# Performance work log

Measured on AMD Instinct MI355X. Metric: run time of the kernel, lower is better.

## Reference

```python
import jax, jax.numpy as jnp
import numpy as np

N_NODES = 100000
N_EDGES = 1600000
IN_F = 128
OUT_F = 32


def setup_inputs() -> dict:
    key = jax.random.key(0)
    k1, k2, k3, k4, k5, k6 = jax.random.split(key, 6)
    x = jax.random.normal(k1, (N_NODES, IN_F), dtype=jnp.float32)
    adj_row = jax.random.randint(k2, (N_EDGES,), 0, N_NODES, dtype=jnp.int64)
    adj_col = jax.random.randint(k3, (N_EDGES,), 0, N_NODES, dtype=jnp.int64)
    adj_val = jax.random.uniform(k4, (N_EDGES,), dtype=jnp.float32)
    weight = jax.random.normal(k5, (IN_F, OUT_F), dtype=jnp.float32) * (1.0 / np.sqrt(IN_F))
    bias = jax.random.normal(k6, (OUT_F,), dtype=jnp.float32)
    return {"x": x, "adj_row": adj_row, "adj_col": adj_col,
            "adj_val": adj_val, "weight": weight, "bias": bias}


def reference(x, adj_row, adj_col, adj_val, weight, bias):
    # support = input @ W   -> [N, out]
    support = x @ weight
    # spmm(adj, support): out[r] = sum_e val[e] * support[col[e]] for edges with row[e]==r
    gathered = adj_val[:, None] * support[adj_col]  # [E, out]
    out = jax.ops.segment_sum(gathered, adj_row, num_segments=N_NODES)
    return out + bias
```

## Files before the change

kernel.cpp:

```cpp
#include <hip/hip_runtime.h>
#include <stdint.h>

#define N_NODES 100000
#define N_EDGES 1600000
#define IN_F 128
#define OUT_F 32

#define RB 64
#define NB 1563
#define ABLK 256
#define EPA (N_EDGES / ABLK)
#define NTOT (NB * ABLK)
#define NSA NB
#define CAP 1536
#define MTILES (N_NODES / 16)
#define GEMM_BLKS ((MTILES + 7) / 8)

typedef __attribute__((ext_vector_type(8))) short bf16x8;
typedef __attribute__((ext_vector_type(4))) float f32x4;

__device__ __forceinline__ float bf2f(unsigned short u) {
    return __uint_as_float(((uint32_t)u) << 16);
}
__device__ __forceinline__ unsigned short f2bf(float x) {
    const uint32_t b = __float_as_uint(x);
    return (unsigned short)((b + 0x7fffu + ((b >> 16) & 1u)) >> 16);
}

__global__ __launch_bounds__(512) void gcn_gemm_count(const float* __restrict__ x,
                                                      const float* __restrict__ w,
                                                      unsigned short* __restrict__ support,
                                                      const int* __restrict__ row,
                                                      int* __restrict__ count) {
    __shared__ unsigned short wt[OUT_F][IN_F + 8];
    __shared__ int h[NB];
    const int tid = threadIdx.x;

    if (blockIdx.x < GEMM_BLKS) {
        #pragma unroll
        for (int i = tid; i < IN_F * OUT_F; i += 512) {
            const int k = i >> 5, f = i & 31;
            wt[f][k] = f2bf(w[i]);
        }
        __syncthreads();

        const int wv = tid >> 6;
        const int lane = tid & 63;
        const int rowT = blockIdx.x * 8 + wv;
        if (rowT >= MTILES) return;
        const int row0 = rowT * 16;

        const int mrow = lane & 15;
        const int kg = lane >> 4;
        const int kb = kg * 8;

        bf16x8 bfrag[4][2];
        #pragma unroll
        for (int ks = 0; ks < 4; ++ks) {
            #pragma unroll
            for (int nt = 0; nt < 2; ++nt) {
                bfrag[ks][nt] = *reinterpret_cast<const bf16x8*>(
                    &wt[mrow + nt * 16][ks * 32 + kb]);
            }
        }

        f32x4 acc0 = {0.f, 0.f, 0.f, 0.f};
        f32x4 acc1 = {0.f, 0.f, 0.f, 0.f};
        const float* xr = &x[(size_t)(row0 + mrow) * IN_F];
        #pragma unroll
        for (int ks = 0; ks < 4; ++ks) {
            const float4 a0 = *reinterpret_cast<const float4*>(&xr[ks * 32 + kb]);
            const float4 a1 = *reinterpret_cast<const float4*>(&xr[ks * 32 + kb + 4]);
            bf16x8 af;
            af[0] = (short)f2bf(a0.x); af[1] = (short)f2bf(a0.y);
            af[2] = (short)f2bf(a0.z); af[3] = (short)f2bf(a0.w);
            af[4] = (short)f2bf(a1.x); af[5] = (short)f2bf(a1.y);
            af[6] = (short)f2bf(a1.z); af[7] = (short)f2bf(a1.w);
            acc0 = __builtin_amdgcn_mfma_f32_16x16x32_bf16(af, bfrag[ks][0], acc0, 0, 0, 0);
            acc1 = __builtin_amdgcn_mfma_f32_16x16x32_bf16(af, bfrag[ks][1], acc1, 0, 0, 0);
        }
        #pragma unroll
        for (int r = 0; r < 4; ++r) {
            const int orow = row0 + kg * 4 + r;
            support[(size_t)orow * OUT_F + mrow]      = f2bf(acc0[r]);
            support[(size_t)orow * OUT_F + mrow + 16] = f2bf(acc1[r]);
        }
    } else {
        const int b = blockIdx.x - GEMM_BLKS;
        for (int i = tid; i < NB; i += 512) h[i] = 0;
        __syncthreads();
        const int e0 = b * EPA;
        for (int i = tid; i < EPA; i += 512)
            atomicAdd(&h[row[e0 + i] >> 6], 1);
        __syncthreads();
        for (int i = tid; i < NB; i += 512)
            count[i * ABLK + b] = h[i];
    }
}

__global__ __launch_bounds__(256) void scan_a(const int* __restrict__ count,
                                              int* __restrict__ ptr,
                                              int* __restrict__ bsum) {
    __shared__ int s[256];
    const int i = blockIdx.x * 256 + threadIdx.x;
    const int v = count[i];
    s[threadIdx.x] = v;
    __syncthreads();
    for (int off = 1; off < 256; off <<= 1) {
        const int t = (threadIdx.x >= off) ? s[threadIdx.x - off] : 0;
        __syncthreads();
        s[threadIdx.x] += t;
        __syncthreads();
    }
    ptr[i] = s[threadIdx.x] - v;
    if (threadIdx.x == 255) bsum[blockIdx.x] = s[255];
}

__global__ __launch_bounds__(1024) void scan_b(int* __restrict__ bsum) {
    __shared__ int s[1024];
    const int t = threadIdx.x;
    const int v0 = (2 * t     < NSA) ? bsum[2 * t]     : 0;
    const int v1 = (2 * t + 1 < NSA) ? bsum[2 * t + 1] : 0;
    const int sum = v0 + v1;
    s[t] = sum;
    __syncthreads();
    for (int off = 1; off < 1024; off <<= 1) {
        const int x = (t >= off) ? s[t - off] : 0;
        __syncthreads();
        s[t] += x;
        __syncthreads();
    }
    const int excl = s[t] - sum;
    if (2 * t     < NSA) bsum[2 * t]     = excl;
    if (2 * t + 1 < NSA) bsum[2 * t + 1] = excl + v0;
}

__global__ __launch_bounds__(1024) void gcn_bin(const int* __restrict__ row,
                                                const int* __restrict__ col,
                                                const float* __restrict__ val,
                                                const int* __restrict__ ptr,
                                                const int* __restrict__ bsum,
                                                long long* __restrict__ rec) {
    __shared__ int cur[NB];
    const int tid = threadIdx.x, b = blockIdx.x;
    for (int i = tid; i < NB; i += 1024)
        cur[i] = bsum[i] + ptr[i * ABLK + b];
    __syncthreads();
    const int e0 = b * EPA;

    int i = tid;
    for (; i + 3 * 1024 < EPA; i += 4 * 1024) {
        const int r0 = row[e0 + i];
        const int r1 = row[e0 + i + 1024];
        const int r2 = row[e0 + i + 2048];
        const int r3 = row[e0 + i + 3072];
        const int c0 = col[e0 + i];
        const int c1 = col[e0 + i + 1024];
        const int c2 = col[e0 + i + 2048];
        const int c3 = col[e0 + i + 3072];
        const uint32_t v0 = __float_as_uint(val[e0 + i]);
        const uint32_t v1 = __float_as_uint(val[e0 + i + 1024]);
        const uint32_t v2 = __float_as_uint(val[e0 + i + 2048]);
        const uint32_t v3 = __float_as_uint(val[e0 + i + 3072]);
        const int s0 = atomicAdd(&cur[r0 >> 6], 1);
        const int s1 = atomicAdd(&cur[r1 >> 6], 1);
        const int s2 = atomicAdd(&cur[r2 >> 6], 1);
        const int s3 = atomicAdd(&cur[r3 >> 6], 1);
        rec[s0] = (long long)(((uint64_t)v0 << 32) |
                  (uint64_t)((uint32_t)c0 | ((uint32_t)(r0 & 63) << 17)));
        rec[s1] = (long long)(((uint64_t)v1 << 32) |
                  (uint64_t)((uint32_t)c1 | ((uint32_t)(r1 & 63) << 17)));
        rec[s2] = (long long)(((uint64_t)v2 << 32) |
                  (uint64_t)((uint32_t)c2 | ((uint32_t)(r2 & 63) << 17)));
        rec[s3] = (long long)(((uint64_t)v3 << 32) |
                  (uint64_t)((uint32_t)c3 | ((uint32_t)(r3 & 63) << 17)));
    }
    for (; i < EPA; i += 1024) {
        const int e = e0 + i;
        const int r = row[e];
        const int slot = atomicAdd(&cur[r >> 6], 1);
        rec[slot] = (long long)(((uint64_t)__float_as_uint(val[e]) << 32) |
                    (uint64_t)((uint32_t)col[e] | ((uint32_t)(r & 63) << 17)));
    }
}

__global__ __launch_bounds__(1024) void gcn_rows(const int* __restrict__ bsum,
                                                 const long long* __restrict__ rec,
                                                 const unsigned short* __restrict__ sup,
                                                 const float* __restrict__ bias,
                                                 float* __restrict__ out) {
    __shared__ long long rbuf[CAP];
    __shared__ long long srt[CAP];
    __shared__ int cnt[RB];
    __shared__ int rs[RB + 1];
    __shared__ float bs[OUT_F];
    const int tid = threadIdx.x, k = blockIdx.x;

    const int start = bsum[k];
    const int end = (k < NB - 1) ? bsum[k + 1] : N_EDGES;
    const int span = end - start;
    const int n = min(span, CAP);

    if (tid < OUT_F) bs[tid] = bias[tid];
    if (tid < RB) cnt[tid] = 0;
    for (int i = tid; i < n; i += 1024) rbuf[i] = rec[start + i];
    __syncthreads();

    for (int i = tid; i < n; i += 1024)
        atomicAdd(&cnt[(int)(((uint64_t)rbuf[i] >> 17) & 63)], 1);
    __syncthreads();

    if (tid < 64) {
        const int v = cnt[tid];
        int sc = v;
        #pragma unroll
        for (int d = 1; d < 64; d <<= 1) {
            const int t2 = __shfl_up(sc, d, 64);
            if (tid >= d) sc += t2;
        }
        rs[tid] = sc - v;
        cnt[tid] = sc - v;
        if (tid == 63) rs[64] = sc;
    }
    __syncthreads();

    for (int i = tid; i < n; i += 1024) {
        const long long pk = rbuf[i];
        const int rl = (int)(((uint64_t)pk >> 17) & 63);
        const int slot = atomicAdd(&cnt[rl], 1);
        srt[slot] = pk;
    }
    __syncthreads();

    const int g = tid >> 5;
    const int f = tid & 31;
    const int rowBase = k * RB;

    for (int rp = 0; rp < 2; ++rp) {
        const int r = rp * 32 + g;
        const int gr = rowBase + r;
        const int s0 = rs[r];
        const int s1 = rs[r + 1];
        float a0 = bs[f], a1 = 0.f, a2 = 0.f, a3 = 0.f;
        int i = s0;
        for (; i + 4 <= s1; i += 4) {
            const uint64_t p0 = (uint64_t)srt[i];
            const uint64_t p1 = (uint64_t)srt[i + 1];
            const uint64_t p2 = (uint64_t)srt[i + 2];
            const uint64_t p3 = (uint64_t)srt[i + 3];
            const unsigned short q0 = sup[(size_t)(p0 & 0x1ffff) * OUT_F + f];
            const unsigned short q1 = sup[(size_t)(p1 & 0x1ffff) * OUT_F + f];
            const unsigned short q2 = sup[(size_t)(p2 & 0x1ffff) * OUT_F + f];
            const unsigned short q3 = sup[(size_t)(p3 & 0x1ffff) * OUT_F + f];
            a0 += __uint_as_float((uint32_t)(p0 >> 32)) * bf2f(q0);
            a1 += __uint_as_float((uint32_t)(p1 >> 32)) * bf2f(q1);
            a2 += __uint_as_float((uint32_t)(p2 >> 32)) * bf2f(q2);
            a3 += __uint_as_float((uint32_t)(p3 >> 32)) * bf2f(q3);
        }
        for (; i < s1; ++i) {
            const uint64_t pk = (uint64_t)srt[i];
            const unsigned short q = sup[(size_t)(pk & 0x1ffff) * OUT_F + f];
            a0 += __uint_as_float((uint32_t)(pk >> 32)) * bf2f(q);
        }
        for (int j = CAP; j < span; ++j) {
            const uint64_t pk = (uint64_t)rec[start + j];
            if ((int)((pk >> 17) & 63) == r) {
                const unsigned short q = sup[(size_t)(pk & 0x1ffff) * OUT_F + f];
                a0 += __uint_as_float((uint32_t)(pk >> 32)) * bf2f(q);
            }
        }
        if (gr < N_NODES)
            out[(size_t)gr * OUT_F + f] = (a0 + a1) + (a2 + a3);
    }
}

__global__ __launch_bounds__(256) void gcn_bias_init(const float* __restrict__ bias,
                                                     float* __restrict__ out) {
    const int i = blockIdx.x * 256 + threadIdx.x;
    if (i < N_NODES * OUT_F) out[i] = bias[i & 31];
}

__global__ __launch_bounds__(256) void gcn_scatter(const int* __restrict__ row,
                                                   const int* __restrict__ col,
                                                   const float* __restrict__ val,
                                                   const unsigned short* __restrict__ sup,
                                                   float* __restrict__ out) {
    const int f = threadIdx.x & 31;
    const int grp = threadIdx.x >> 5;
    long long e = (long long)blockIdx.x * 8 + grp;
    const long long stride = (long long)gridDim.x * 8;
    for (; e < N_EDGES; e += stride) {
        const int r = row[e];
        const int c = col[e];
        const float v = val[e];
        const float s = bf2f(sup[(size_t)c * OUT_F + f]);
        atomicAdd(&out[(size_t)r * OUT_F + f], v * s);
    }
}

extern "C" void kernel_launch(void* const* d_in, const int* in_sizes, int n_in,
                              void* d_out, int out_size, void* d_ws, size_t ws_size,
                              hipStream_t stream) {
    const float* x       = (const float*)d_in[0];
    const int*   adj_row = (const int*)d_in[1];
    const int*   adj_col = (const int*)d_in[2];
    const float* adj_val = (const float*)d_in[3];
    const float* weight  = (const float*)d_in[4];
    const float* bias    = (const float*)d_in[5];
    float* out = (float*)d_out;

    char* ws = (char*)d_ws;
    const size_t SUPPORT_B = (((size_t)N_NODES * OUT_F * 2) + 255) & ~(size_t)255;
    const size_t REC_B     = (size_t)N_EDGES * 8;
    const size_t CNT_B     = ((size_t)NTOT * 4 + 255) & ~(size_t)255;
    const size_t BSUM_B    = ((size_t)NSA * 4 + 255) & ~(size_t)255;
    const size_t NEED = SUPPORT_B + REC_B + 2 * CNT_B + BSUM_B;

    unsigned short* support = (unsigned short*)(ws);
    long long* rec  = (long long*)(ws + SUPPORT_B);
    int* count      = (int*)(ws + SUPPORT_B + REC_B);
    int* ptr        = (int*)(ws + SUPPORT_B + REC_B + CNT_B);
    int* bsum       = (int*)(ws + SUPPORT_B + REC_B + 2 * CNT_B);

    if (ws_size >= NEED) {
        gcn_gemm_count<<<GEMM_BLKS + ABLK, 512, 0, stream>>>(x, weight, support,
                                                             adj_row, count);
        scan_a<<<NSA, 256, 0, stream>>>(count, ptr, bsum);
        scan_b<<<1, 1024, 0, stream>>>(bsum);
        gcn_bin<<<ABLK, 1024, 0, stream>>>(adj_row, adj_col, adj_val, ptr, bsum, rec);
        gcn_rows<<<NB, 1024, 0, stream>>>(bsum, rec, support, bias, out);
    } else {
        gcn_gemm_count<<<GEMM_BLKS, 512, 0, stream>>>(x, weight, support,
                                                      adj_row, (int*)ws);
        gcn_bias_init<<<(N_NODES * OUT_F + 255) / 256, 256, 0, stream>>>(bias, out);
        gcn_scatter<<<8192, 256, 0, stream>>>(adj_row, adj_col, adj_val, support, out);
    }
}
```

Measured before the change: 83.59 us.

## Replace count-scan-bin pipeline with fixed-capacity buckets and fused binning

Drops the global per-block count matrix, the two-level prefix scan and the separate binning kernel. Each row bucket now gets a fixed CAP-sized region, and the GEMM/count kernel reserves slots per bucket with one global atomic per bucket per block, then writes records directly. Records that exceed the capacity go to an overflow list that every row block scans. This cuts launches and the extra passes over row/col/val. In exchange it uses more workspace, and the overflow path costs a linear scan per block if it is ever used.

Measured after the change: 81.80 us. 1.02x faster.

```diff
diff --git a/kernel.cpp b/kernel.cpp
--- a/kernel.cpp
+++ b/kernel.cpp
@@ -10,8 +10,6 @@
 #define NB 1563
 #define ABLK 256
 #define EPA (N_EDGES / ABLK)
-#define NTOT (NB * ABLK)
-#define NSA NB
 #define CAP 1536
 #define MTILES (N_NODES / 16)
 #define GEMM_BLKS ((MTILES + 7) / 8)
@@ -27,11 +25,24 @@
     return (unsigned short)((b + 0x7fffu + ((b >> 16) & 1u)) >> 16);
 }
 
-__global__ __launch_bounds__(512) void gcn_gemm_count(const float* __restrict__ x,
-                                                      const float* __restrict__ w,
-                                                      unsigned short* __restrict__ support,
-                                                      const int* __restrict__ row,
-                                                      int* __restrict__ count) {
+__global__ __launch_bounds__(256) void gcn_init(int* __restrict__ cur,
+                                                int* __restrict__ ovf_cnt) {
+    const int i = blockIdx.x * 256 + threadIdx.x;
+    if (i < NB) cur[i] = i * CAP;
+    if (i == NB) *ovf_cnt = 0;
+}
+
+__global__ __launch_bounds__(512) void gcn_gemm_bin(const float* __restrict__ x,
+                                                    const float* __restrict__ w,
+                                                    unsigned short* __restrict__ support,
+                                                    const int* __restrict__ row,
+                                                    const int* __restrict__ col,
+                                                    const float* __restrict__ val,
+                                                    int* __restrict__ cur,
+                                                    int* __restrict__ ovf_cnt,
+                                                    long long* __restrict__ rec,
+                                                    long long* __restrict__ ovf_pk,
+                                                    int* __restrict__ ovf_bk) {
     __shared__ unsigned short wt[OUT_F][IN_F + 8];
     __shared__ int h[NB];
     const int tid = threadIdx.x;
@@ -93,99 +104,34 @@
         for (int i = tid; i < EPA; i += 512)
             atomicAdd(&h[row[e0 + i] >> 6], 1);
         __syncthreads();
-        for (int i = tid; i < NB; i += 512)
-            count[i * ABLK + b] = h[i];
-    }
-}
-
-__global__ __launch_bounds__(256) void scan_a(const int* __restrict__ count,
-                                              int* __restrict__ ptr,
-                                              int* __restrict__ bsum) {
-    __shared__ int s[256];
-    const int i = blockIdx.x * 256 + threadIdx.x;
-    const int v = count[i];
-    s[threadIdx.x] = v;
-    __syncthreads();
-    for (int off = 1; off < 256; off <<= 1) {
-        const int t = (threadIdx.x >= off) ? s[threadIdx.x - off] : 0;
+        for (int k = tid; k < NB; k += 512) {
+            const int c = h[k];
+            if (c > 0) h[k] = atomicAdd(&cur[k], c);
+        }
         __syncthreads();
-        s[threadIdx.x] += t;
-        __syncthreads();
-    }
-    ptr[i] = s[threadIdx.x] - v;
-    if (threadIdx.x == 255) bsum[blockIdx.x] = s[255];
-}
-
-__global__ __launch_bounds__(1024) void scan_b(int* __restrict__ bsum) {
-    __shared__ int s[1024];
-    const int t = threadIdx.x;
-    const int v0 = (2 * t     < NSA) ? bsum[2 * t]     : 0;
-    const int v1 = (2 * t + 1 < NSA) ? bsum[2 * t + 1] : 0;
-    const int sum = v0 + v1;
-    s[t] = sum;
-    __syncthreads();
-    for (int off = 1; off < 1024; off <<= 1) {
-        const int x = (t >= off) ? s[t - off] : 0;
-        __syncthreads();
-        s[t] += x;
-        __syncthreads();
-    }
-    const int excl = s[t] - sum;
-    if (2 * t     < NSA) bsum[2 * t]     = excl;
-    if (2 * t + 1 < NSA) bsum[2 * t + 1] = excl + v0;
-}
-
-__global__ __launch_bounds__(1024) void gcn_bin(const int* __restrict__ row,
-                                                const int* __restrict__ col,
-                                                const float* __restrict__ val,
-                                                const int* __restrict__ ptr,
-                                                const int* __restrict__ bsum,
-                                                long long* __restrict__ rec) {
-    __shared__ int cur[NB];
-    const int tid = threadIdx.x, b = blockIdx.x;
-    for (int i = tid; i < NB; i += 1024)
-        cur[i] = bsum[i] + ptr[i * ABLK + b];
-    __syncthreads();
-    const int e0 = b * EPA;
-
-    int i = tid;
-    for (; i + 3 * 1024 < EPA; i += 4 * 1024) {
-        const int r0 = row[e0 + i];
-        const int r1 = row[e0 + i + 1024];
-        const int r2 = row[e0 + i + 2048];
-        const int r3 = row[e0 + i + 3072];
-        const int c0 = col[e0 + i];
-        const int c1 = col[e0 + i + 1024];
-        const int c2 = col[e0 + i + 2048];
-        const int c3 = col[e0 + i + 3072];
-        const uint32_t v0 = __float_as_uint(val[e0 + i]);
-        const uint32_t v1 = __float_as_uint(val[e0 + i + 1024]);
-        const uint32_t v2 = __float_as_uint(val[e0 + i + 2048]);
-        const uint32_t v3 = __float_as_uint(val[e0 + i + 3072]);
-        const int s0 = atomicAdd(&cur[r0 >> 6], 1);
-        const int s1 = atomicAdd(&cur[r1 >> 6], 1);
-        const int s2 = atomicAdd(&cur[r2 >> 6], 1);
-        const int s3 = atomicAdd(&cur[r3 >> 6], 1);
-        rec[s0] = (long long)(((uint64_t)v0 << 32) |
-                  (uint64_t)((uint32_t)c0 | ((uint32_t)(r0 & 63) << 17)));
-        rec[s1] = (long long)(((uint64_t)v1 << 32) |
-                  (uint64_t)((uint32_t)c1 | ((uint32_t)(r1 & 63) << 17)));
-        rec[s2] = (long long)(((uint64_t)v2 << 32) |
-                  (uint64_t)((uint32_t)c2 | ((uint32_t)(r2 & 63) << 17)));
-        rec[s3] = (long long)(((uint64_t)v3 << 32) |
-                  (uint64_t)((uint32_t)c3 | ((uint32_t)(r3 & 63) << 17)));
-    }
-    for (; i < EPA; i += 1024) {
-        const int e = e0 + i;
-        const int r = row[e];
-        const int slot = atomicAdd(&cur[r >> 6], 1);
-        rec[slot] = (long long)(((uint64_t)__float_as_uint(val[e]) << 32) |
-                    (uint64_t)((uint32_t)col[e] | ((uint32_t)(r & 63) << 17)));
-    }
-}
-
-__global__ __launch_bounds__(1024) void gcn_rows(const int* __restrict__ bsum,
+        for (int i = tid; i < EPA; i += 512) {
+            const int e = e0 + i;
+            const int r = row[e];
+            const int k = r >> 6;
+            const int slot = atomicAdd(&h[k], 1);
+            const long long pk = (long long)(((uint64_t)__float_as_uint(val[e]) << 32) |
+                      (uint64_t)((uint32_t)col[e] | ((uint32_t)(r & 63) << 17)));
+            if (slot < (k + 1) * CAP) {
+                rec[slot] = pk;
+            } else {
+                const int oi = atomicAdd(ovf_cnt, 1);
+                ovf_pk[oi] = pk;
+                ovf_bk[oi] = k;
+            }
+        }
+    }
+}
+
+__global__ __launch_bounds__(1024) void gcn_rows(const int* __restrict__ cur,
+                                                 const int* __restrict__ ovf_cnt,
                                                  const long long* __restrict__ rec,
+                                                 const long long* __restrict__ ovf_pk,
+                                                 const int* __restrict__ ovf_bk,
                                                  const unsigned short* __restrict__ sup,
                                                  const float* __restrict__ bias,
                                                  float* __restrict__ out) {
@@ -196,10 +142,10 @@
     __shared__ float bs[OUT_F];
     const int tid = threadIdx.x, k = blockIdx.x;
 
-    const int start = bsum[k];
-    const int end = (k < NB - 1) ? bsum[k + 1] : N_EDGES;
-    const int span = end - start;
-    const int n = min(span, CAP);
+    const int start = k * CAP;
+    const int total = cur[k] - start;
+    const int n = min(total, CAP);
+    const int novf = *ovf_cnt;
 
     if (tid < OUT_F) bs[tid] = bias[tid];
     if (tid < RB) cnt[tid] = 0;
@@ -262,11 +208,13 @@
             const unsigned short q = sup[(size_t)(pk & 0x1ffff) * OUT_F + f];
             a0 += __uint_as_float((uint32_t)(pk >> 32)) * bf2f(q);
         }
-        for (int j = CAP; j < span; ++j) {
-            const uint64_t pk = (uint64_t)rec[start + j];
-            if ((int)((pk >> 17) & 63) == r) {
-                const unsigned short q = sup[(size_t)(pk & 0x1ffff) * OUT_F + f];
-                a0 += __uint_as_float((uint32_t)(pk >> 32)) * bf2f(q);
+        for (int j = 0; j < novf; ++j) {
+            if (ovf_bk[j] == k) {
+                const uint64_t pk = (uint64_t)ovf_pk[j];
+                if ((int)((pk >> 17) & 63) == r) {
+                    const unsigned short q = sup[(size_t)(pk & 0x1ffff) * OUT_F + f];
+                    a0 += __uint_as_float((uint32_t)(pk >> 32)) * bf2f(q);
+                }
             }
         }
         if (gr < N_NODES)
@@ -278,6 +226,55 @@
                                                      float* __restrict__ out) {
     const int i = blockIdx.x * 256 + threadIdx.x;
     if (i < N_NODES * OUT_F) out[i] = bias[i & 31];
+}
+
+__global__ __launch_bounds__(512) void gcn_gemm_only(const float* __restrict__ x,
+                                                     const float* __restrict__ w,
+                                                     unsigned short* __restrict__ support) {
+    __shared__ unsigned short wt[OUT_F][IN_F + 8];
+    const int tid = threadIdx.x;
+    #pragma unroll
+    for (int i = tid; i < IN_F * OUT_F; i += 512) {
+        const int k = i >> 5, f = i & 31;
+        wt[f][k] = f2bf(w[i]);
+    }
+    __syncthreads();
+    const int wv = tid >> 6;
+    const int lane = tid & 63;
+    const int rowT = blockIdx.x * 8 + wv;
+    if (rowT >= MTILES) return;
+    const int row0 = rowT * 16;
+    const int mrow = lane & 15;
+    const int kg = lane >> 4;
+    const int kb = kg * 8;
+    bf16x8 bfrag[4][2];
+    #pragma unroll
+    for (int ks = 0; ks < 4; ++ks)
+        #pragma unroll
+        for (int nt = 0; nt < 2; ++nt)
+            bfrag[ks][nt] = *reinterpret_cast<const bf16x8*>(
+                &wt[mrow + nt * 16][ks * 32 + kb]);
+    f32x4 acc0 = {0.f, 0.f, 0.f, 0.f};
+    f32x4 acc1 = {0.f, 0.f, 0.f, 0.f};
+    const float* xr = &x[(size_t)(row0 + mrow) * IN_F];
+    #pragma unroll
+    for (int ks = 0; ks < 4; ++ks) {
+        const float4 a0 = *reinterpret_cast<const float4*>(&xr[ks * 32 + kb]);
+        const float4 a1 = *reinterpret_cast<const float4*>(&xr[ks * 32 + kb + 4]);
+        bf16x8 af;
+        af[0] = (short)f2bf(a0.x); af[1] = (short)f2bf(a0.y);
+        af[2] = (short)f2bf(a0.z); af[3] = (short)f2bf(a0.w);
+        af[4] = (short)f2bf(a1.x); af[5] = (short)f2bf(a1.y);
+        af[6] = (short)f2bf(a1.z); af[7] = (short)f2bf(a1.w);
+        acc0 = __builtin_amdgcn_mfma_f32_16x16x32_bf16(af, bfrag[ks][0], acc0, 0, 0, 0);
+        acc1 = __builtin_amdgcn_mfma_f32_16x16x32_bf16(af, bfrag[ks][1], acc1, 0, 0, 0);
+    }
+    #pragma unroll
+    for (int r = 0; r < 4; ++r) {
+        const int orow = row0 + kg * 4 + r;
+        support[(size_t)orow * OUT_F + mrow]      = f2bf(acc0[r]);
+        support[(size_t)orow * OUT_F + mrow + 16] = f2bf(acc1[r]);
+    }
 }
 
 __global__ __launch_bounds__(256) void gcn_scatter(const int* __restrict__ row,
@@ -311,27 +308,30 @@
 
     char* ws = (char*)d_ws;
     const size_t SUPPORT_B = (((size_t)N_NODES * OUT_F * 2) + 255) & ~(size_t)255;
-    const size_t REC_B     = (size_t)N_EDGES * 8;
-    const size_t CNT_B     = ((size_t)NTOT * 4 + 255) & ~(size_t)255;
-    const size_t BSUM_B    = ((size_t)NSA * 4 + 255) & ~(size_t)255;
-    const size_t NEED = SUPPORT_B + REC_B + 2 * CNT_B + BSUM_B;
+    const size_t REC_B     = (((size_t)NB * CAP * 8) + 255) & ~(size_t)255;
+    const size_t CUR_B     = (((size_t)NB * 4) + 255) & ~(size_t)255;
+    const size_t OCN_B     = 256;
+    const size_t OPK_B     = (size_t)N_EDGES * 8;
+    const size_t OBK_B     = (size_t)N_EDGES * 4;
+    const size_t NEED = SUPPORT_B + REC_B + CUR_B + OCN_B + OPK_B + OBK_B;
 
     unsigned short* support = (unsigned short*)(ws);
     long long* rec  = (long long*)(ws + SUPPORT_B);
-    int* count      = (int*)(ws + SUPPORT_B + REC_B);
-    int* ptr        = (int*)(ws + SUPPORT_B + REC_B + CNT_B);
-    int* bsum       = (int*)(ws + SUPPORT_B + REC_B + 2 * CNT_B);
+    int* cur        = (int*)(ws + SUPPORT_B + REC_B);
+    int* ovf_cnt    = (int*)(ws + SUPPORT_B + REC_B + CUR_B);
+    long long* ovf_pk = (long long*)(ws + SUPPORT_B + REC_B + CUR_B + OCN_B);
+    int* ovf_bk     = (int*)(ws + SUPPORT_B + REC_B + CUR_B + OCN_B + OPK_B);
 
     if (ws_size >= NEED) {
-        gcn_gemm_count<<<GEMM_BLKS + ABLK, 512, 0, stream>>>(x, weight, support,
-                                                             adj_row, count);
-        scan_a<<<NSA, 256, 0, stream>>>(count, ptr, bsum);
-        scan_b<<<1, 1024, 0, stream>>>(bsum);
-        gcn_bin<<<ABLK, 1024, 0, stream>>>(adj_row, adj_col, adj_val, ptr, bsum, rec);
-        gcn_rows<<<NB, 1024, 0, stream>>>(bsum, rec, support, bias, out);
+        gcn_init<<<(NB + 256) / 256, 256, 0, stream>>>(cur, ovf_cnt);
+        gcn_gemm_bin<<<GEMM_BLKS + ABLK, 512, 0, stream>>>(x, weight, support,
+                                                           adj_row, adj_col, adj_val,
+                                                           cur, ovf_cnt, rec,
+                                                           ovf_pk, ovf_bk);
+        gcn_rows<<<NB, 1024, 0, stream>>>(cur, ovf_cnt, rec, ovf_pk, ovf_bk,
+                                          support, bias, out);
     } else {
-        gcn_gemm_count<<<GEMM_BLKS, 512, 0, stream>>>(x, weight, support,
-                                                      adj_row, (int*)ws);
+        gcn_gemm_only<<<GEMM_BLKS, 512, 0, stream>>>(x, weight, support);
         gcn_bias_init<<<(N_NODES * OUT_F + 255) / 256, 256, 0, stream>>>(bias, out);
         gcn_scatter<<<8192, 256, 0, stream>>>(adj_row, adj_col, adj_val, support, out);
     }
```
